# Optimization experiments

Hardware: AMD Instinct MI355X
Metric: run time of the kernel (lower is better)

Reference implementation:

```python
import jax, jax.numpy as jnp
import numpy as np

P = 4  # patch_size


def setup_inputs() -> dict:
    key = jax.random.key(0)
    ks = jax.random.split(key, 5)
    B, H, W, C = 4, 256, 256, 256
    x = jax.random.normal(ks[0], (B, H, W, C), dtype=jnp.float32)
    scale = 1.0 / np.sqrt(C)
    Wq = jax.random.normal(ks[1], (C, C), dtype=jnp.float32) * scale
    bq = jax.random.normal(ks[2], (C,), dtype=jnp.float32) * 0.01
    Wo = jax.random.normal(ks[3], (C, C), dtype=jnp.float32) * scale
    bo = jax.random.normal(ks[4], (C,), dtype=jnp.float32) * 0.01
    return {"x": x, "Wq": Wq, "bq": bq, "Wo": Wo, "bo": bo}


def reference(x, Wq, bq, Wo, bo):
    p = P
    ps = p * p
    B, h, w, C = x.shape
    q_h, r_h = h // ps, (h % ps) // 2
    q_w, r_w = w // ps, (w % ps) // 2
    # centered crop to a multiple of p_square (identity when divisible)
    x = x[:, r_h:q_h * ps + r_h, r_w:q_w * ps + r_w, :]
    nH, nW = q_h * p, q_w * p  # number of p x p windows per axis
    # window partition: [B, nH, p, nW, p, C] -> [B, nH, nW, p*p, C]
    xw = x.reshape(B, nH, p, nW, p, C).transpose(0, 1, 3, 2, 4, 5)
    xw = xw.reshape(B, nH, nW, ps, C)
    # NOTE: source uses self.query for Q, K, and V (key/value layers unused)
    q = xw @ Wq.T + bq  # [B, nH, nW, p*p, C]
    scores = jnp.einsum('bhwic,bhwjc->bhwij', q, q)  # unscaled, per source
    attn = jax.nn.softmax(scores, axis=-1)
    z = jnp.einsum('bhwij,bhwjc->bhwic', attn, q)
    return z @ Wo.T + bo  # [B, nH, nW, p*p, C]
```

## Files before the change

kernel.cpp:

```cpp
#include <hip/hip_runtime.h>


typedef __attribute__((ext_vector_type(8))) short short8;
typedef __attribute__((ext_vector_type(4))) short short4v;
typedef __attribute__((ext_vector_type(4))) float floatx4;

#define MFMA32(a, b, c) __builtin_amdgcn_mfma_f32_16x16x32_bf16(a, b, c, 0, 0, 0)
#define MFMA16(a, b, c) __builtin_amdgcn_mfma_f32_16x16x16bf16_1k(a, b, c, 0, 0, 0)

static __device__ inline short f2bf(float f) {
    unsigned u = __float_as_uint(f);
    u = (u + 0x7FFFu + ((u >> 16) & 1u)) >> 16;
    return (short)u;
}
static __device__ inline floatx4 zf4() {
    floatx4 v;
#pragma unroll
    for (int k = 0; k < 4; ++k) v[k] = 0.0f;
    return v;
}
static __device__ inline short8 cvt8(float4 v0, float4 v1) {
    short8 a;
    a[0] = f2bf(v0.x); a[1] = f2bf(v0.y); a[2] = f2bf(v0.z); a[3] = f2bf(v0.w);
    a[4] = f2bf(v1.x); a[5] = f2bf(v1.y); a[6] = f2bf(v1.z); a[7] = f2bf(v1.w);
    return a;
}
static __device__ inline short4v pack4(floatx4 a) {
    short4v r;
    r[0] = f2bf(a[0]); r[1] = f2bf(a[1]); r[2] = f2bf(a[2]); r[3] = f2bf(a[3]);
    return r;
}
static __device__ inline short4v pack4b(floatx4 a, float4 b) {
    short4v r;
    r[0] = f2bf(a[0] + b.x); r[1] = f2bf(a[1] + b.y);
    r[2] = f2bf(a[2] + b.z); r[3] = f2bf(a[3] + b.w);
    return r;
}

__global__ void convert_weights(const float* __restrict__ Wq,
                                const float* __restrict__ Wo,
                                short* __restrict__ wbf) {
    int idx = blockIdx.x * 256 + threadIdx.x;
    int n = idx >> 8, k = idx & 255;
    wbf[idx] = f2bf(Wq[idx]);
    int kk = k >> 4, q4 = (k >> 2) & 3, r = k & 3;
    int pk = (kk >> 1) * 32 + q4 * 8 + (kk & 1) * 4 + r;
    wbf[65536 + n * 256 + pk] = f2bf(Wo[idx]);
}

__global__ __launch_bounds__(256, 3) void lsa_fused(
    const float* __restrict__ x, const short* __restrict__ wbf,
    const float* __restrict__ bq, const float* __restrict__ bo,
    float* __restrict__ out) {
    const int tid  = threadIdx.x;
    const int wv   = tid >> 6;
    const int lane = tid & 63;
    const int l15  = lane & 15;
    const int quad = lane >> 4;

    const int wid0 = (blockIdx.x * 4 + wv) * 2;
    const int pi = l15 >> 2, pj = l15 & 3;

    const float* xrow[2];
#pragma unroll
    for (int w = 0; w < 2; ++w) {
        int wid = wid0 + w;
        int b = wid >> 12, hp = (wid >> 6) & 63, wp = wid & 63;
        xrow[w] = x + ((size_t)b << 24) + ((size_t)((hp << 2) + pi) << 16)
                    + ((size_t)((wp << 2) + pj) << 8);
    }

    short8 xf[2][8];
#pragma unroll
    for (int w = 0; w < 2; ++w)
#pragma unroll
        for (int kk = 0; kk < 8; ++kk) {
            const float* p = xrow[w] + kk * 32 + quad * 8;
            float4 v0 = *(const float4*)p;
            float4 v1 = *(const float4*)(p + 4);
            xf[w][kk] = cvt8(v0, v1);
        }

    short4v qf[2][16];
#pragma unroll 2
    for (int nt = 0; nt < 16; ++nt) {
        floatx4 a0 = zf4(), a1 = zf4();
        const short* wq = wbf + (nt * 16 + l15) * 256 + quad * 8;
#pragma unroll
        for (int kk = 0; kk < 8; ++kk) {
            short8 wf = *(const short8*)(wq + kk * 32);
            a0 = MFMA32(wf, xf[0][kk], a0);
            a1 = MFMA32(wf, xf[1][kk], a1);
        }
        float4 b4 = *(const float4*)(bq + nt * 16 + quad * 4);
        qf[0][nt] = pack4b(a0, b4);
        qf[1][nt] = pack4b(a1, b4);
    }

    floatx4 s0 = zf4(), s1 = zf4();
#pragma unroll
    for (int nt = 0; nt < 16; ++nt) {
        s0 = MFMA16(qf[0][nt], qf[0][nt], s0);
        s1 = MFMA16(qf[1][nt], qf[1][nt], s1);
    }

    short4v paf[2];
#pragma unroll
    for (int w = 0; w < 2; ++w) {
        floatx4 s = w ? s1 : s0;
        float m = fmaxf(fmaxf(s[0], s[1]), fmaxf(s[2], s[3]));
        m = fmaxf(m, __shfl_xor(m, 16, 64));
        m = fmaxf(m, __shfl_xor(m, 32, 64));
        float e0 = __expf(s[0] - m), e1 = __expf(s[1] - m);
        float e2 = __expf(s[2] - m), e3 = __expf(s[3] - m);
        float sum = (e0 + e1) + (e2 + e3);
        sum += __shfl_xor(sum, 16, 64);
        sum += __shfl_xor(sum, 32, 64);
        float inv = 1.0f / sum;
        short4v pf;
        pf[0] = f2bf(e0 * inv); pf[1] = f2bf(e1 * inv);
        pf[2] = f2bf(e2 * inv); pf[3] = f2bf(e3 * inv);
        paf[w] = pf;
    }

    short4v idf;
#pragma unroll
    for (int j = 0; j < 4; ++j) idf[j] = (l15 == quad * 4 + j) ? (short)0x3F80 : (short)0;

    float* o0p = out + (size_t)wid0 * 4096;
    float* o1p = o0p + 4096;

#pragma unroll 2
    for (int nt = 0; nt < 16; ++nt) {
        floatx4 y0 = zf4(), y1 = zf4();
        const short* wo = wbf + 65536 + (nt * 16 + l15) * 256 + quad * 8;
#pragma unroll
        for (int kk2 = 0; kk2 < 8; ++kk2) {
            short8 wf = *(const short8*)(wo + kk2 * 32);
            short4v wlo, whi;
            wlo[0] = wf[0]; wlo[1] = wf[1]; wlo[2] = wf[2]; wlo[3] = wf[3];
            whi[0] = wf[4]; whi[1] = wf[5]; whi[2] = wf[6]; whi[3] = wf[7];
            y0 = MFMA16(wlo, qf[0][2 * kk2], y0);
            y1 = MFMA16(wlo, qf[1][2 * kk2], y1);
            y0 = MFMA16(whi, qf[0][2 * kk2 + 1], y0);
            y1 = MFMA16(whi, qf[1][2 * kk2 + 1], y1);
        }
        floatx4 t0 = MFMA16(pack4(y0), idf, zf4());
        floatx4 t1 = MFMA16(pack4(y1), idf, zf4());
        floatx4 o0 = MFMA16(paf[0], pack4(t0), zf4());
        floatx4 o1 = MFMA16(paf[1], pack4(t1), zf4());
        float bov = bo[nt * 16 + l15];
#pragma unroll
        for (int r = 0; r < 4; ++r) {
            o0p[(quad * 4 + r) * 256 + nt * 16 + l15] = o0[r] + bov;
            o1p[(quad * 4 + r) * 256 + nt * 16 + l15] = o1[r] + bov;
        }
    }
}

extern "C" void kernel_launch(void* const* d_in, const int* in_sizes, int n_in,
                              void* d_out, int out_size, void* d_ws, size_t ws_size,
                              hipStream_t stream) {
    const float* x  = (const float*)d_in[0];
    const float* Wq = (const float*)d_in[1];
    const float* bq = (const float*)d_in[2];
    const float* Wo = (const float*)d_in[3];
    const float* bo = (const float*)d_in[4];
    float* out = (float*)d_out;
    short* wbf = (short*)d_ws;

    hipLaunchKernelGGL(convert_weights, dim3(256), dim3(256), 0, stream, Wq, Wo, wbf);
    hipLaunchKernelGGL(lsa_fused, dim3(2048), dim3(256), 0, stream,
                       x, wbf, bq, bo, out);
}
```

Measured before the change: 645.3 us.

## Process one window per wave, split K accumulators, and store output with float4

```diff
diff --git a/kernel.cpp b/kernel.cpp
--- a/kernel.cpp
+++ b/kernel.cpp
@@ -30,10 +30,10 @@
     r[0] = f2bf(a[0]); r[1] = f2bf(a[1]); r[2] = f2bf(a[2]); r[3] = f2bf(a[3]);
     return r;
 }
-static __device__ inline short4v pack4b(floatx4 a, float4 b) {
+static __device__ inline short4v pack4sb(floatx4 a, floatx4 b, float4 c) {
     short4v r;
-    r[0] = f2bf(a[0] + b.x); r[1] = f2bf(a[1] + b.y);
-    r[2] = f2bf(a[2] + b.z); r[3] = f2bf(a[3] + b.w);
+    r[0] = f2bf(a[0] + b[0] + c.x); r[1] = f2bf(a[1] + b[1] + c.y);
+    r[2] = f2bf(a[2] + b[2] + c.z); r[3] = f2bf(a[3] + b[3] + c.w);
     return r;
 }
 
@@ -48,7 +48,7 @@
     wbf[65536 + n * 256 + pk] = f2bf(Wo[idx]);
 }
 
-__global__ __launch_bounds__(256, 3) void lsa_fused(
+__global__ __launch_bounds__(256, 4) void lsa_fused(
     const float* __restrict__ x, const short* __restrict__ wbf,
     const float* __restrict__ bq, const float* __restrict__ bo,
     float* __restrict__ out) {
@@ -58,77 +58,63 @@
     const int l15  = lane & 15;
     const int quad = lane >> 4;
 
-    const int wid0 = (blockIdx.x * 4 + wv) * 2;
+    const int wid = blockIdx.x * 4 + wv;
     const int pi = l15 >> 2, pj = l15 & 3;
+    const int b = wid >> 12, hp = (wid >> 6) & 63, wp = wid & 63;
+    const float* xrow = x + ((size_t)b << 24) + ((size_t)((hp << 2) + pi) << 16)
+                          + ((size_t)((wp << 2) + pj) << 8);
 
-    const float* xrow[2];
+    short8 xf[8];
 #pragma unroll
-    for (int w = 0; w < 2; ++w) {
-        int wid = wid0 + w;
-        int b = wid >> 12, hp = (wid >> 6) & 63, wp = wid & 63;
-        xrow[w] = x + ((size_t)b << 24) + ((size_t)((hp << 2) + pi) << 16)
-                    + ((size_t)((wp << 2) + pj) << 8);
+    for (int kk = 0; kk < 8; ++kk) {
+        const float* p = xrow + kk * 32 + quad * 8;
+        float4 v0 = *(const float4*)p;
+        float4 v1 = *(const float4*)(p + 4);
+        xf[kk] = cvt8(v0, v1);
     }
 
-    short8 xf[2][8];
-#pragma unroll
-    for (int w = 0; w < 2; ++w)
-#pragma unroll
-        for (int kk = 0; kk < 8; ++kk) {
-            const float* p = xrow[w] + kk * 32 + quad * 8;
-            float4 v0 = *(const float4*)p;
-            float4 v1 = *(const float4*)(p + 4);
-            xf[w][kk] = cvt8(v0, v1);
-        }
-
-    short4v qf[2][16];
+    short4v qf[16];
 #pragma unroll 2
     for (int nt = 0; nt < 16; ++nt) {
         floatx4 a0 = zf4(), a1 = zf4();
         const short* wq = wbf + (nt * 16 + l15) * 256 + quad * 8;
 #pragma unroll
-        for (int kk = 0; kk < 8; ++kk) {
-            short8 wf = *(const short8*)(wq + kk * 32);
-            a0 = MFMA32(wf, xf[0][kk], a0);
-            a1 = MFMA32(wf, xf[1][kk], a1);
+        for (int kk = 0; kk < 4; ++kk) {
+            short8 w0 = *(const short8*)(wq + kk * 64);
+            short8 w1 = *(const short8*)(wq + kk * 64 + 32);
+            a0 = MFMA32(w0, xf[2 * kk], a0);
+            a1 = MFMA32(w1, xf[2 * kk + 1], a1);
         }
         float4 b4 = *(const float4*)(bq + nt * 16 + quad * 4);
-        qf[0][nt] = pack4b(a0, b4);
-        qf[1][nt] = pack4b(a1, b4);
+        qf[nt] = pack4sb(a0, a1, b4);
     }
 
-    floatx4 s0 = zf4(), s1 = zf4();
+    floatx4 sa = zf4(), sb = zf4();
 #pragma unroll
-    for (int nt = 0; nt < 16; ++nt) {
-        s0 = MFMA16(qf[0][nt], qf[0][nt], s0);
-        s1 = MFMA16(qf[1][nt], qf[1][nt], s1);
+    for (int h = 0; h < 8; ++h) {
+        sa = MFMA16(qf[2 * h], qf[2 * h], sa);
+        sb = MFMA16(qf[2 * h + 1], qf[2 * h + 1], sb);
     }
+    floatx4 s = sa + sb;
 
-    short4v paf[2];
-#pragma unroll
-    for (int w = 0; w < 2; ++w) {
-        floatx4 s = w ? s1 : s0;
-        float m = fmaxf(fmaxf(s[0], s[1]), fmaxf(s[2], s[3]));
-        m = fmaxf(m, __shfl_xor(m, 16, 64));
-        m = fmaxf(m, __shfl_xor(m, 32, 64));
-        float e0 = __expf(s[0] - m), e1 = __expf(s[1] - m);
-        float e2 = __expf(s[2] - m), e3 = __expf(s[3] - m);
-        float sum = (e0 + e1) + (e2 + e3);
-        sum += __shfl_xor(sum, 16, 64);
-        sum += __shfl_xor(sum, 32, 64);
-        float inv = 1.0f / sum;
-        short4v pf;
-        pf[0] = f2bf(e0 * inv); pf[1] = f2bf(e1 * inv);
-        pf[2] = f2bf(e2 * inv); pf[3] = f2bf(e3 * inv);
-        paf[w] = pf;
-    }
+    float m = fmaxf(fmaxf(s[0], s[1]), fmaxf(s[2], s[3]));
+    m = fmaxf(m, __shfl_xor(m, 16, 64));
+    m = fmaxf(m, __shfl_xor(m, 32, 64));
+    float e0 = __expf(s[0] - m), e1 = __expf(s[1] - m);
+    float e2 = __expf(s[2] - m), e3 = __expf(s[3] - m);
+    float sum = (e0 + e1) + (e2 + e3);
+    sum += __shfl_xor(sum, 16, 64);
+    sum += __shfl_xor(sum, 32, 64);
+    float inv = 1.0f / sum;
+    short4v paf;
+    paf[0] = f2bf(e0 * inv); paf[1] = f2bf(e1 * inv);
+    paf[2] = f2bf(e2 * inv); paf[3] = f2bf(e3 * inv);
 
     short4v idf;
 #pragma unroll
     for (int j = 0; j < 4; ++j) idf[j] = (l15 == quad * 4 + j) ? (short)0x3F80 : (short)0;
 
-    float* o0p = out + (size_t)wid0 * 4096;
-    float* o1p = o0p + 4096;
+    float* op = out + (size_t)wid * 4096 + l15 * 256;
 
 #pragma unroll 2
     for (int nt = 0; nt < 16; ++nt) {
@@ -140,21 +126,17 @@
             short4v wlo, whi;
             wlo[0] = wf[0]; wlo[1] = wf[1]; wlo[2] = wf[2]; wlo[3] = wf[3];
             whi[0] = wf[4]; whi[1] = wf[5]; whi[2] = wf[6]; whi[3] = wf[7];
-            y0 = MFMA16(wlo, qf[0][2 * kk2], y0);
-            y1 = MFMA16(wlo, qf[1][2 * kk2], y1);
-            y0 = MFMA16(whi, qf[0][2 * kk2 + 1], y0);
-            y1 = MFMA16(whi, qf[1][2 * kk2 + 1], y1);
+            y0 = MFMA16(wlo, qf[2 * kk2], y0);
+            y1 = MFMA16(whi, qf[2 * kk2 + 1], y1);
         }
-        floatx4 t0 = MFMA16(pack4(y0), idf, zf4());
-        floatx4 t1 = MFMA16(pack4(y1), idf, zf4());
-        floatx4 o0 = MFMA16(paf[0], pack4(t0), zf4());
-        floatx4 o1 = MFMA16(paf[1], pack4(t1), zf4());
-        float bov = bo[nt * 16 + l15];
-#pragma unroll
-        for (int r = 0; r < 4; ++r) {
-            o0p[(quad * 4 + r) * 256 + nt * 16 + l15] = o0[r] + bov;
-            o1p[(quad * 4 + r) * 256 + nt * 16 + l15] = o1[r] + bov;
-        }
+        floatx4 y = y0 + y1;
+        floatx4 t = MFMA16(pack4(y), idf, zf4());
+        floatx4 oT = MFMA16(pack4(t), paf, zf4());
+        float4 bo4 = *(const float4*)(bo + nt * 16 + quad * 4);
+        float4 st;
+        st.x = oT[0] + bo4.x; st.y = oT[1] + bo4.y;
+        st.z = oT[2] + bo4.z; st.w = oT[3] + bo4.w;
+        *(float4*)(op + nt * 16 + quad * 4) = st;
     }
 }
 
@@ -170,6 +152,6 @@
     short* wbf = (short*)d_ws;
 
     hipLaunchKernelGGL(convert_weights, dim3(256), dim3(256), 0, stream, Wq, Wo, wbf);
-    hipLaunchKernelGGL(lsa_fused, dim3(2048), dim3(256), 0, stream,
+    hipLaunchKernelGGL(lsa_fused, dim3(4096), dim3(256), 0, stream,
                        x, wbf, bq, bo, out);
 }
```

Measured after the change: 871.7 us. 35.1% more time.

## Stage swizzled bf16 weights through double-buffered LDS via async global-to-LDS loads

Applied to the files above, without the earlier changes.

```diff
diff --git a/kernel.cpp b/kernel.cpp
--- a/kernel.cpp
+++ b/kernel.cpp
@@ -7,6 +7,9 @@
 
 #define MFMA32(a, b, c) __builtin_amdgcn_mfma_f32_16x16x32_bf16(a, b, c, 0, 0, 0)
 #define MFMA16(a, b, c) __builtin_amdgcn_mfma_f32_16x16x16bf16_1k(a, b, c, 0, 0, 0)
+
+typedef __attribute__((address_space(1))) const unsigned int GU32;
+typedef __attribute__((address_space(3))) unsigned int LU32;
 
 static __device__ inline short f2bf(float f) {
     unsigned u = __float_as_uint(f);
@@ -30,10 +33,10 @@
     r[0] = f2bf(a[0]); r[1] = f2bf(a[1]); r[2] = f2bf(a[2]); r[3] = f2bf(a[3]);
     return r;
 }
-static __device__ inline short4v pack4b(floatx4 a, float4 b) {
+static __device__ inline short4v pack4b(floatx4 a, float4 c) {
     short4v r;
-    r[0] = f2bf(a[0] + b.x); r[1] = f2bf(a[1] + b.y);
-    r[2] = f2bf(a[2] + b.z); r[3] = f2bf(a[3] + b.w);
+    r[0] = f2bf(a[0] + c.x); r[1] = f2bf(a[1] + c.y);
+    r[2] = f2bf(a[2] + c.z); r[3] = f2bf(a[3] + c.w);
     return r;
 }
 
@@ -41,22 +44,41 @@
                                 const float* __restrict__ Wo,
                                 short* __restrict__ wbf) {
     int idx = blockIdx.x * 256 + threadIdx.x;
-    int n = idx >> 8, k = idx & 255;
-    wbf[idx] = f2bf(Wq[idx]);
+    int row = idx >> 8, k = idx & 255;
+    int rr = row & 31, c = row >> 5;
+    int swz = (rr & 7) << 4;
+
+    int offq = (rr * 512 + k * 2) ^ swz;
+    wbf[(c * 16384 + offq) >> 1] = f2bf(Wq[idx]);
+
     int kk = k >> 4, q4 = (k >> 2) & 3, r = k & 3;
     int pk = (kk >> 1) * 32 + q4 * 8 + (kk & 1) * 4 + r;
-    wbf[65536 + n * 256 + pk] = f2bf(Wo[idx]);
+    int offo = (rr * 512 + pk * 2) ^ swz;
+    wbf[(131072 + c * 16384 + offo) >> 1] = f2bf(Wo[idx]);
 }
 
 __global__ __launch_bounds__(256, 3) void lsa_fused(
     const float* __restrict__ x, const short* __restrict__ wbf,
     const float* __restrict__ bq, const float* __restrict__ bo,
     float* __restrict__ out) {
+    __shared__ __align__(16) short lds[2][8192];
+
     const int tid  = threadIdx.x;
     const int wv   = tid >> 6;
     const int lane = tid & 63;
     const int l15  = lane & 15;
     const int quad = lane >> 4;
+    const int swz  = (l15 & 7) << 4;
+
+#define STAGE(b, g)                                                            \
+    do {                                                                       \
+        const short* _src = wbf + (size_t)(g) * 8192 + tid * 8;                \
+        short* _dst = &lds[b][tid * 8];                                        \
+        _Pragma("unroll") for (int _i = 0; _i < 4; ++_i)                       \
+            __builtin_amdgcn_global_load_lds((GU32*)(_src + _i * 2048),        \
+                                             (LU32*)(_dst + _i * 2048),        \
+                                             16, 0, 0);                        \
+    } while (0)
 
     const int wid0 = (blockIdx.x * 4 + wv) * 2;
     const int pi = l15 >> 2, pj = l15 & 3;
@@ -69,6 +91,8 @@
         xrow[w] = x + ((size_t)b << 24) + ((size_t)((hp << 2) + pi) << 16)
                     + ((size_t)((wp << 2) + pj) << 8);
     }
+
+    STAGE(0, 0);
 
     short8 xf[2][8];
 #pragma unroll
@@ -81,33 +105,45 @@
             xf[w][kk] = cvt8(v0, v1);
         }
 
+    __syncthreads();
+
     short4v qf[2][16];
-#pragma unroll 2
-    for (int nt = 0; nt < 16; ++nt) {
-        floatx4 a0 = zf4(), a1 = zf4();
-        const short* wq = wbf + (nt * 16 + l15) * 256 + quad * 8;
-#pragma unroll
-        for (int kk = 0; kk < 8; ++kk) {
-            short8 wf = *(const short8*)(wq + kk * 32);
-            a0 = MFMA32(wf, xf[0][kk], a0);
-            a1 = MFMA32(wf, xf[1][kk], a1);
+    const int lbase = l15 * 512 + quad * 16;
+#pragma unroll 1
+    for (int c = 0; c < 8; ++c) {
+        STAGE((c + 1) & 1, c + 1);
+        const char* Lb = (const char*)&lds[c & 1][0];
+#pragma unroll
+        for (int h = 0; h < 2; ++h) {
+            const int nt = c * 2 + h;
+            floatx4 a0 = zf4(), a1 = zf4();
+            const int base = lbase + h * 8192;
+#pragma unroll
+            for (int kk = 0; kk < 8; ++kk) {
+                short8 wf = *(const short8*)(Lb + ((base + kk * 64) ^ swz));
+                a0 = MFMA32(wf, xf[0][kk], a0);
+                a1 = MFMA32(wf, xf[1][kk], a1);
+            }
+            float4 b4 = *(const float4*)(bq + nt * 16 + quad * 4);
+            qf[0][nt] = pack4b(a0, b4);
+            qf[1][nt] = pack4b(a1, b4);
         }
-        float4 b4 = *(const float4*)(bq + nt * 16 + quad * 4);
-        qf[0][nt] = pack4b(a0, b4);
-        qf[1][nt] = pack4b(a1, b4);
-    }
-
-    floatx4 s0 = zf4(), s1 = zf4();
-#pragma unroll
-    for (int nt = 0; nt < 16; ++nt) {
-        s0 = MFMA16(qf[0][nt], qf[0][nt], s0);
-        s1 = MFMA16(qf[1][nt], qf[1][nt], s1);
+        __syncthreads();
+    }
+
+    floatx4 s0a = zf4(), s0b = zf4(), s1a = zf4(), s1b = zf4();
+#pragma unroll
+    for (int h = 0; h < 8; ++h) {
+        s0a = MFMA16(qf[0][2 * h], qf[0][2 * h], s0a);
+        s0b = MFMA16(qf[0][2 * h + 1], qf[0][2 * h + 1], s0b);
+        s1a = MFMA16(qf[1][2 * h], qf[1][2 * h], s1a);
+        s1b = MFMA16(qf[1][2 * h + 1], qf[1][2 * h + 1], s1b);
     }
 
     short4v paf[2];
 #pragma unroll
     for (int w = 0; w < 2; ++w) {
-        floatx4 s = w ? s1 : s0;
+        floatx4 s = w ? (s1a + s1b) : (s0a + s0b);
         float m = fmaxf(fmaxf(s[0], s[1]), fmaxf(s[2], s[3]));
         m = fmaxf(m, __shfl_xor(m, 16, 64));
         m = fmaxf(m, __shfl_xor(m, 32, 64));
@@ -127,35 +163,45 @@
 #pragma unroll
     for (int j = 0; j < 4; ++j) idf[j] = (l15 == quad * 4 + j) ? (short)0x3F80 : (short)0;
 
-    float* o0p = out + (size_t)wid0 * 4096;
-    float* o1p = o0p + 4096;
-
-#pragma unroll 2
-    for (int nt = 0; nt < 16; ++nt) {
-        floatx4 y0 = zf4(), y1 = zf4();
-        const short* wo = wbf + 65536 + (nt * 16 + l15) * 256 + quad * 8;
-#pragma unroll
-        for (int kk2 = 0; kk2 < 8; ++kk2) {
-            short8 wf = *(const short8*)(wo + kk2 * 32);
-            short4v wlo, whi;
-            wlo[0] = wf[0]; wlo[1] = wf[1]; wlo[2] = wf[2]; wlo[3] = wf[3];
-            whi[0] = wf[4]; whi[1] = wf[5]; whi[2] = wf[6]; whi[3] = wf[7];
-            y0 = MFMA16(wlo, qf[0][2 * kk2], y0);
-            y1 = MFMA16(wlo, qf[1][2 * kk2], y1);
-            y0 = MFMA16(whi, qf[0][2 * kk2 + 1], y0);
-            y1 = MFMA16(whi, qf[1][2 * kk2 + 1], y1);
+    float* op0 = out + (size_t)wid0 * 4096 + l15 * 256;
+    float* op1 = op0 + 4096;
+
+#pragma unroll 1
+    for (int c = 0; c < 8; ++c) {
+        if (c < 7) STAGE((c + 1) & 1, 9 + c);
+        const char* Lb = (const char*)&lds[c & 1][0];
+#pragma unroll
+        for (int h = 0; h < 2; ++h) {
+            const int nt = c * 2 + h;
+            floatx4 y00 = zf4(), y01 = zf4(), y10 = zf4(), y11 = zf4();
+            const int base = lbase + h * 8192;
+#pragma unroll
+            for (int kk2 = 0; kk2 < 8; ++kk2) {
+                short8 wf = *(const short8*)(Lb + ((base + kk2 * 64) ^ swz));
+                short4v wlo, whi;
+                wlo[0] = wf[0]; wlo[1] = wf[1]; wlo[2] = wf[2]; wlo[3] = wf[3];
+                whi[0] = wf[4]; whi[1] = wf[5]; whi[2] = wf[6]; whi[3] = wf[7];
+                y00 = MFMA16(wlo, qf[0][2 * kk2], y00);
+                y10 = MFMA16(wlo, qf[1][2 * kk2], y10);
+                y01 = MFMA16(whi, qf[0][2 * kk2 + 1], y01);
+                y11 = MFMA16(whi, qf[1][2 * kk2 + 1], y11);
+            }
+            floatx4 t0 = MFMA16(pack4(y00 + y01), idf, zf4());
+            floatx4 t1 = MFMA16(pack4(y10 + y11), idf, zf4());
+            floatx4 o0 = MFMA16(pack4(t0), paf[0], zf4());
+            floatx4 o1 = MFMA16(pack4(t1), paf[1], zf4());
+            float4 bo4 = *(const float4*)(bo + nt * 16 + quad * 4);
+            float4 r0, r1;
+            r0.x = o0[0] + bo4.x; r0.y = o0[1] + bo4.y;
+            r0.z = o0[2] + bo4.z; r0.w = o0[3] + bo4.w;
+            r1.x = o1[0] + bo4.x; r1.y = o1[1] + bo4.y;
+            r1.z = o1[2] + bo4.z; r1.w = o1[3] + bo4.w;
+            *(float4*)(op0 + nt * 16 + quad * 4) = r0;
+            *(float4*)(op1 + nt * 16 + quad * 4) = r1;
         }
-        floatx4 t0 = MFMA16(pack4(y0), idf, zf4());
-        floatx4 t1 = MFMA16(pack4(y1), idf, zf4());
-        floatx4 o0 = MFMA16(paf[0], pack4(t0), zf4());
-        floatx4 o1 = MFMA16(paf[1], pack4(t1), zf4());
-        float bov = bo[nt * 16 + l15];
-#pragma unroll
-        for (int r = 0; r < 4; ++r) {
-            o0p[(quad * 4 + r) * 256 + nt * 16 + l15] = o0[r] + bov;
-            o1p[(quad * 4 + r) * 256 + nt * 16 + l15] = o1[r] + bov;
-        }
-    }
+        __syncthreads();
+    }
+#undef STAGE
 }
 
 extern "C" void kernel_launch(void* const* d_in, const int* in_sizes, int n_in,
```

Result: slower. 698.2 us (+8.2%).
